# Performance work log

Measured on AMD Instinct MI355X. Metric: run time of the kernel, lower is better.

Reference implementation:

```python
import jax, jax.numpy as jnp
import numpy as np

STAGES = [80, 40, 20]
INPUT = 640
NUM_CLASSES = 80
B = 32
PRE_NMS = 1000      # top-k candidates fed to NMS (fixed-shape surrogate for full sort)
MAX_DET = 100       # max_num_detections
IOU_TH = 0.5
CLASS_OFF = 4096.0  # batched_nms trick: offset boxes per class so classes never overlap


def setup_inputs() -> dict:
    key = jax.random.key(0)
    ks = jax.random.split(key, 6)
    inp = {}
    for i, s in enumerate(STAGES):
        inp[f"cls{i}"] = jax.random.normal(ks[2 * i], (B, NUM_CLASSES, s, s), dtype=jnp.float32)
        # positive ltrb distances, up to ~64 px
        inp[f"box{i}"] = jax.random.uniform(ks[2 * i + 1], (B, 4, s, s), dtype=jnp.float32) * 64.0
    return inp


def _decode_level(cls, box, stage):
    # cls: [B,C,H,W], box: [B,4,H,W]
    step = INPUT // stage
    cls = jax.nn.sigmoid(jnp.transpose(cls, (0, 2, 3, 1)))   # [B,H,W,C]
    conf = jnp.max(cls, axis=-1)                             # [B,H,W]
    cidx = jnp.argmax(cls, axis=-1)                          # [B,H,W]
    box = jnp.transpose(box, (0, 2, 3, 1))                   # [B,H,W,4]
    grid = jnp.arange(stage, dtype=box.dtype) * step
    gx, gy = jnp.meshgrid(grid, grid, indexing='xy')
    block = jnp.stack([gx, gy], axis=-1)                     # [H,W,2]
    xy1 = block - box[..., :2]
    xy2 = block + box[..., 2:4]
    boxes = jnp.concatenate([xy1, xy2], axis=-1).reshape(box.shape[0], -1, 4)
    return boxes, conf.reshape(conf.shape[0], -1), cidx.reshape(cidx.shape[0], -1)


def _iou_matrix(b):
    # b: [N,4] -> [N,N] pairwise IoU
    area = jnp.maximum(b[:, 2] - b[:, 0], 0.) * jnp.maximum(b[:, 3] - b[:, 1], 0.)
    lt = jnp.maximum(b[:, None, :2], b[None, :, :2])
    rb = jnp.minimum(b[:, None, 2:], b[None, :, 2:])
    wh = jnp.maximum(rb - lt, 0.)
    inter = wh[..., 0] * wh[..., 1]
    return inter / (area[:, None] + area[None, :] - inter + 1e-7)


def _nms_image(boxes, scores, classes):
    # class-aware (batched) NMS via per-class coordinate offset
    off = classes.astype(boxes.dtype) * CLASS_OFF
    ob = boxes + off[:, None]
    s_top, idx = jax.lax.top_k(scores, PRE_NMS)
    b_top = ob[idx]                                          # [PRE,4], score-sorted desc
    iou = _iou_matrix(b_top)
    ar = jnp.arange(PRE_NMS)

    def body(i, supp):
        row = (iou[i] > IOU_TH) & (ar > i)
        return jnp.where(supp[i], supp, supp | row)

    supp = jax.lax.fori_loop(0, PRE_NMS, body, jnp.zeros((PRE_NMS,), bool))
    kept_scores = jnp.where(supp, -jnp.inf, s_top)
    sel_s, sel = jax.lax.top_k(kept_scores, MAX_DET)
    final = idx[sel]                                         # indices into original 8400
    valid = jnp.isfinite(sel_s)
    out_b = jnp.where(valid[:, None], boxes[final], 0.)
    out_s = jnp.where(valid, scores[final], 0.)
    out_c = jnp.where(valid, classes[final], -1)
    return out_b, out_s, out_c


def reference(cls0, box0, cls1, box1, cls2, box2):
    parts = [_decode_level(c, b, s) for c, b, s in
             zip([cls0, cls1, cls2], [box0, box1, box2], STAGES)]
    boxes = jnp.concatenate([p[0] for p in parts], axis=1)    # [B,8400,4]
    scores = jnp.concatenate([p[1] for p in parts], axis=1)   # [B,8400]
    classes = jnp.concatenate([p[2] for p in parts], axis=1)  # [B,8400]
    ob, os_, oc = jax.vmap(_nms_image)(boxes, scores, classes)
    boxes_with_scores = jnp.concatenate([ob, os_[..., None]], axis=-1)  # [B,MAX_DET,5]
    return boxes_with_scores, oc
```

## Files before the change

### kernel.cpp

```cpp
#include <hip/hip_runtime.h>

typedef unsigned int u32;
typedef unsigned long long u64;

#define NB 32
#define NCLS 80
#define NANCHOR 8400
#define PRE 1000
#define MAXDET 100
#define NT 1024

__global__ void decode_kernel(const float* __restrict__ cls0, const float* __restrict__ box0,
                              const float* __restrict__ cls1, const float* __restrict__ box1,
                              const float* __restrict__ cls2, const float* __restrict__ box2,
                              float* __restrict__ ws_scores, float4* __restrict__ ws_boxes,
                              int* __restrict__ ws_cls) {
    int g = blockIdx.x * blockDim.x + threadIdx.x;
    if (g >= NB * NANCHOR) return;
    int b = g / NANCHOR;
    int r = g - b * NANCHOR;

    const float* cp; const float* bp;
    int HW, hw, h, w, step;
    if (r < 6400) {
        cp = cls0 + (size_t)b * NCLS * 6400; bp = box0 + (size_t)b * 4 * 6400;
        HW = 6400; hw = r;        h = hw / 80; w = hw - h * 80; step = 8;
    } else if (r < 8000) {
        cp = cls1 + (size_t)b * NCLS * 1600; bp = box1 + (size_t)b * 4 * 1600;
        HW = 1600; hw = r - 6400; h = hw / 40; w = hw - h * 40; step = 16;
    } else {
        cp = cls2 + (size_t)b * NCLS * 400;  bp = box2 + (size_t)b * 4 * 400;
        HW = 400;  hw = r - 8000; h = hw / 20; w = hw - h * 20; step = 32;
    }

    float m = cp[hw];
    int ci = 0;
    for (int c = 1; c < NCLS; ++c) {
        float v = cp[(size_t)c * HW + hw];
        if (v > m) { m = v; ci = c; }
    }
    float score = 1.0f / (1.0f + expf(-m));

    float l = bp[hw], t = bp[HW + hw], rr = bp[2 * HW + hw], bo = bp[3 * HW + hw];
    float gx = (float)(w * step), gy = (float)(h * step);

    ws_scores[g] = score;
    ws_boxes[g] = make_float4(gx - l, gy - t, gx + rr, gy + bo);
    ws_cls[g] = ci;
}

__global__ __launch_bounds__(NT) void nms_kernel(const float* __restrict__ ws_scores,
                                                 const float4* __restrict__ ws_boxes,
                                                 const int* __restrict__ ws_cls,
                                                 float* __restrict__ out) {
    const int b = blockIdx.x;
    const int tid = threadIdx.x;

    __shared__ int s_hist[1024];
    __shared__ u64 s_key[2048];
    __shared__ float s_x1[PRE], s_y1[PRE], s_x2[PRE], s_y2[PRE], s_area[PRE];
    __shared__ int s_supp[PRE];
    __shared__ int s_keep[MAXDET];
    __shared__ int s_C, s_base;
    __shared__ u32 s_thresh;
    __shared__ int s_cnt;

    const float* sc = ws_scores + (size_t)b * NANCHOR;

    s_hist[tid] = 0;
    __syncthreads();
    for (int a = tid; a < NANCHOR; a += NT) {
        u32 sb = __float_as_uint(sc[a]);
        atomicAdd(&s_hist[sb >> 20], 1);
    }
    __syncthreads();
    for (int off = 1; off < 1024; off <<= 1) {
        int v = s_hist[tid];
        int u = (tid + off < 1024) ? s_hist[tid + off] : 0;
        __syncthreads();
        s_hist[tid] = v + u;
        __syncthreads();
    }
    {
        int sfx = s_hist[tid];
        int nxt = (tid < 1023) ? s_hist[tid + 1] : 0;
        if (sfx >= PRE && (tid == 1023 || nxt < PRE)) { s_C = tid; s_base = nxt; }
    }
    __syncthreads();
    const int C = s_C, base = s_base;
    __syncthreads();

    s_hist[tid] = 0;
    __syncthreads();
    for (int a = tid; a < NANCHOR; a += NT) {
        u32 sb = __float_as_uint(sc[a]);
        if ((int)(sb >> 20) == C) atomicAdd(&s_hist[(sb >> 10) & 1023], 1);
    }
    __syncthreads();
    for (int off = 1; off < 1024; off <<= 1) {
        int v = s_hist[tid];
        int u = (tid + off < 1024) ? s_hist[tid + off] : 0;
        __syncthreads();
        s_hist[tid] = v + u;
        __syncthreads();
    }
    {
        int sfx = base + s_hist[tid];
        int nxt = base + ((tid < 1023) ? s_hist[tid + 1] : 0);
        if (sfx >= PRE && (tid == 1023 || nxt < PRE))
            s_thresh = ((u32)C << 20) | ((u32)tid << 10);
    }
    if (tid == 0) s_cnt = 0;
    s_key[tid] = 0ULL;
    s_key[tid + 1024] = 0ULL;
    __syncthreads();
    const u32 thresh = s_thresh;

    for (int a = tid; a < NANCHOR; a += NT) {
        u32 sb = __float_as_uint(sc[a]);
        if (sb >= thresh) {
            int pos = atomicAdd(&s_cnt, 1);
            if (pos < 2048)
                s_key[pos] = ((u64)sb << 14) | (u64)(NANCHOR - 1 - a);
        }
    }
    __syncthreads();

    for (int k = 2; k <= 2048; k <<= 1) {
        for (int j = k >> 1; j > 0; j >>= 1) {
            for (int i = tid; i < 2048; i += NT) {
                int ixj = i ^ j;
                if (ixj > i) {
                    u64 va = s_key[i], vb = s_key[ixj];
                    bool desc = ((i & k) == 0);
                    if (desc ? (va < vb) : (va > vb)) { s_key[i] = vb; s_key[ixj] = va; }
                }
            }
            __syncthreads();
        }
    }

    if (tid < PRE) {
        u64 key = s_key[tid];
        int idx = (NANCHOR - 1) - (int)(key & 16383ULL);
        float4 bx = ws_boxes[(size_t)b * NANCHOR + idx];
        int c = ws_cls[(size_t)b * NANCHOR + idx];
        float off = (float)c * 4096.0f;
        float x1 = bx.x + off, y1 = bx.y + off, x2 = bx.z + off, y2 = bx.w + off;
        s_x1[tid] = x1; s_y1[tid] = y1; s_x2[tid] = x2; s_y2[tid] = y2;
        s_area[tid] = fmaxf(x2 - x1, 0.0f) * fmaxf(y2 - y1, 0.0f);
        s_supp[tid] = 0;
    }
    __syncthreads();

    int nkept = 0;
    for (int i = 0; i < PRE; ++i) {
        if (s_supp[i]) continue;
        if (tid == 0) s_keep[nkept] = i;
        nkept++;
        if (nkept >= MAXDET) break;
        float xi1 = s_x1[i], yi1 = s_y1[i], xi2 = s_x2[i], yi2 = s_y2[i], ai = s_area[i];
        int j = i + 1 + tid;
        if (j < PRE && !s_supp[j]) {
            float lx = fmaxf(xi1, s_x1[j]);
            float ly = fmaxf(yi1, s_y1[j]);
            float rx = fminf(xi2, s_x2[j]);
            float ry = fminf(yi2, s_y2[j]);
            float wx = fmaxf(rx - lx, 0.0f);
            float wy = fmaxf(ry - ly, 0.0f);
            float inter = wx * wy;
            float iou = inter / (ai + s_area[j] - inter + 1e-7f);
            if (iou > 0.5f) s_supp[j] = 1;
        }
        __syncthreads();
    }
    __syncthreads();

    if (tid < MAXDET) {
        float* o = out + ((size_t)b * MAXDET + tid) * 5;
        float* oc = out + (size_t)NB * MAXDET * 5 + (size_t)b * MAXDET + tid;
        if (tid < nkept) {
            int i = s_keep[tid];
            u64 key = s_key[i];
            int idx = (NANCHOR - 1) - (int)(key & 16383ULL);
            float score = __uint_as_float((u32)(key >> 14));
            float4 bx = ws_boxes[(size_t)b * NANCHOR + idx];
            int c = ws_cls[(size_t)b * NANCHOR + idx];
            o[0] = bx.x; o[1] = bx.y; o[2] = bx.z; o[3] = bx.w; o[4] = score;
            *oc = (float)c;
        } else {
            o[0] = 0.0f; o[1] = 0.0f; o[2] = 0.0f; o[3] = 0.0f; o[4] = 0.0f;
            *oc = -1.0f;
        }
    }
}

extern "C" void kernel_launch(void* const* d_in, const int* in_sizes, int n_in,
                              void* d_out, int out_size, void* d_ws, size_t ws_size,
                              hipStream_t stream) {
    const float* cls0 = (const float*)d_in[0];
    const float* box0 = (const float*)d_in[1];
    const float* cls1 = (const float*)d_in[2];
    const float* box1 = (const float*)d_in[3];
    const float* cls2 = (const float*)d_in[4];
    const float* box2 = (const float*)d_in[5];

    float* ws = (float*)d_ws;
    float* ws_scores = ws;
    float4* ws_boxes = (float4*)(ws + NB * NANCHOR);
    int* ws_cls = (int*)(ws + (size_t)NB * NANCHOR * 5);

    int total = NB * NANCHOR;
    decode_kernel<<<(total + 255) / 256, 256, 0, stream>>>(
        cls0, box0, cls1, box1, cls2, box2, ws_scores, ws_boxes, ws_cls);

    nms_kernel<<<NB, NT, 0, stream>>>(ws_scores, ws_boxes, ws_cls, (float*)d_out);
}
```

Baseline: 205.6 us.

## Split decode class reduction across waves and run NMS in one register-resident wave

The decode kernel now gives each 64-anchor group a 256-thread block, with each wave reducing 20 classes before a shared-memory merge. This raises parallelism for the argmax over 80 classes. The NMS kernel drops to 256 threads and keeps scores in registers across the radix-select passes, replacing the log-step block scans with wave-shuffle suffix scans. The greedy suppression loop runs in a single wave with candidate boxes in registers and suppression bits exchanged by shuffles, removing a block barrier per iteration. The trade-off is a smaller block, so the bitonic sort and the other parallel phases do more serial work per thread.

```diff
diff --git a/kernel.cpp b/kernel.cpp
--- a/kernel.cpp
+++ b/kernel.cpp
@@ -8,127 +8,189 @@
 #define NANCHOR 8400
 #define PRE 1000
 #define MAXDET 100
-#define NT 1024
-
-__global__ void decode_kernel(const float* __restrict__ cls0, const float* __restrict__ box0,
-                              const float* __restrict__ cls1, const float* __restrict__ box1,
-                              const float* __restrict__ cls2, const float* __restrict__ box2,
-                              float* __restrict__ ws_scores, float4* __restrict__ ws_boxes,
-                              int* __restrict__ ws_cls) {
-    int g = blockIdx.x * blockDim.x + threadIdx.x;
-    if (g >= NB * NANCHOR) return;
-    int b = g / NANCHOR;
-    int r = g - b * NANCHOR;
+#define NTH 256
+
+__global__ __launch_bounds__(256) void decode_kernel(
+        const float* __restrict__ cls0, const float* __restrict__ box0,
+        const float* __restrict__ cls1, const float* __restrict__ box1,
+        const float* __restrict__ cls2, const float* __restrict__ box2,
+        float* __restrict__ ws_scores, float4* __restrict__ ws_boxes,
+        int* __restrict__ ws_cls) {
+    const int blk = blockIdx.x;
+    const int b = blk / 132;
+    const int ab = blk - b * 132;
+    const int a0 = ab * 64;
+    const int lane = threadIdx.x & 63;
+    const int wv = threadIdx.x >> 6;
 
     const float* cp; const float* bp;
-    int HW, hw, h, w, step;
-    if (r < 6400) {
+    int HW, W, step, hw0;
+    if (a0 < 6400) {
         cp = cls0 + (size_t)b * NCLS * 6400; bp = box0 + (size_t)b * 4 * 6400;
-        HW = 6400; hw = r;        h = hw / 80; w = hw - h * 80; step = 8;
-    } else if (r < 8000) {
+        HW = 6400; W = 80; step = 8;  hw0 = a0;
+    } else if (a0 < 8000) {
         cp = cls1 + (size_t)b * NCLS * 1600; bp = box1 + (size_t)b * 4 * 1600;
-        HW = 1600; hw = r - 6400; h = hw / 40; w = hw - h * 40; step = 16;
+        HW = 1600; W = 40; step = 16; hw0 = a0 - 6400;
     } else {
         cp = cls2 + (size_t)b * NCLS * 400;  bp = box2 + (size_t)b * 4 * 400;
-        HW = 400;  hw = r - 8000; h = hw / 20; w = hw - h * 20; step = 32;
-    }
-
-    float m = cp[hw];
-    int ci = 0;
-    for (int c = 1; c < NCLS; ++c) {
-        float v = cp[(size_t)c * HW + hw];
-        if (v > m) { m = v; ci = c; }
-    }
-    float score = 1.0f / (1.0f + expf(-m));
-
-    float l = bp[hw], t = bp[HW + hw], rr = bp[2 * HW + hw], bo = bp[3 * HW + hw];
-    float gx = (float)(w * step), gy = (float)(h * step);
-
-    ws_scores[g] = score;
-    ws_boxes[g] = make_float4(gx - l, gy - t, gx + rr, gy + bo);
-    ws_cls[g] = ci;
+        HW = 400;  W = 20; step = 32; hw0 = a0 - 8000;
+    }
+
+    const int hw = hw0 + lane;
+    const bool valid = hw < HW;
+
+    __shared__ float s_pm[256];
+    __shared__ int   s_pc[256];
+
+    float m = -1e30f; int ci = 20 * wv;
+    if (valid) {
+        const float* cw = cp + (size_t)(20 * wv) * HW + hw;
+        m = cw[0];
+        #pragma unroll
+        for (int c = 1; c < 20; ++c) {
+            float v = cw[(size_t)c * HW];
+            if (v > m) { m = v; ci = 20 * wv + c; }
+        }
+    }
+    s_pm[threadIdx.x] = m;
+    s_pc[threadIdx.x] = ci;
+    __syncthreads();
+
+    if (threadIdx.x < 64 && valid) {
+        #pragma unroll
+        for (int w = 1; w < 4; ++w) {
+            float v = s_pm[w * 64 + lane];
+            if (v > m) { m = v; ci = s_pc[w * 64 + lane]; }
+        }
+        float score = 1.0f / (1.0f + expf(-m));
+        float l_ = bp[hw], t_ = bp[HW + hw], r_ = bp[2 * HW + hw], bo = bp[3 * HW + hw];
+        int hh = hw / W, ww = hw - hh * W;
+        float gx = (float)(ww * step), gy = (float)(hh * step);
+        int g = b * NANCHOR + a0 + lane;
+        ws_scores[g] = score;
+        ws_boxes[g] = make_float4(gx - l_, gy - t_, gx + r_, gy + bo);
+        ws_cls[g] = ci;
+    }
 }
 
-__global__ __launch_bounds__(NT) void nms_kernel(const float* __restrict__ ws_scores,
-                                                 const float4* __restrict__ ws_boxes,
-                                                 const int* __restrict__ ws_cls,
-                                                 float* __restrict__ out) {
+__device__ __forceinline__ int wave_suffix_incl(int v, int lane) {
+    #pragma unroll
+    for (int off = 1; off < 64; off <<= 1) {
+        int t = __shfl_down(v, off);
+        if (lane + off < 64) v += t;
+    }
+    return v;
+}
+
+__global__ __launch_bounds__(NTH) void nms_kernel(const float* __restrict__ ws_scores,
+                                                  const float4* __restrict__ ws_boxes,
+                                                  const int* __restrict__ ws_cls,
+                                                  float* __restrict__ out) {
     const int b = blockIdx.x;
     const int tid = threadIdx.x;
+    const int lane = tid & 63;
+    const int wv = tid >> 6;
 
     __shared__ int s_hist[1024];
     __shared__ u64 s_key[2048];
-    __shared__ float s_x1[PRE], s_y1[PRE], s_x2[PRE], s_y2[PRE], s_area[PRE];
-    __shared__ int s_supp[PRE];
+    __shared__ float4 s_box[PRE];
+    __shared__ float s_area[PRE];
     __shared__ int s_keep[MAXDET];
+    __shared__ int s_wtot[4];
     __shared__ int s_C, s_base;
     __shared__ u32 s_thresh;
-    __shared__ int s_cnt;
+    __shared__ int s_cnt, s_nkept;
 
     const float* sc = ws_scores + (size_t)b * NANCHOR;
 
-    s_hist[tid] = 0;
-    __syncthreads();
-    for (int a = tid; a < NANCHOR; a += NT) {
-        u32 sb = __float_as_uint(sc[a]);
-        atomicAdd(&s_hist[sb >> 20], 1);
-    }
-    __syncthreads();
-    for (int off = 1; off < 1024; off <<= 1) {
-        int v = s_hist[tid];
-        int u = (tid + off < 1024) ? s_hist[tid + off] : 0;
+    u32 sb[33];
+    #pragma unroll
+    for (int k = 0; k < 33; ++k) {
+        int a = tid + (k << 8);
+        sb[k] = (a < NANCHOR) ? __float_as_uint(sc[a]) : 0u;
+    }
+    *(int4*)&s_hist[4 * tid] = make_int4(0, 0, 0, 0);
+    __syncthreads();
+
+    #pragma unroll
+    for (int k = 0; k < 33; ++k) {
+        int a = tid + (k << 8);
+        if (a < NANCHOR) atomicAdd(&s_hist[sb[k] >> 20], 1);
+    }
+    __syncthreads();
+
+    {
+        int b0 = s_hist[4 * tid], b1 = s_hist[4 * tid + 1], b2 = s_hist[4 * tid + 2], b3 = s_hist[4 * tid + 3];
+        int l3 = b3, l2 = b2 + b3, l1 = b1 + l2, l0 = b0 + l1;
+        int wincl = wave_suffix_incl(l0, lane);
+        if (lane == 0) s_wtot[wv] = wincl;
+        int add = wincl - l0;
         __syncthreads();
-        s_hist[tid] = v + u;
+        #pragma unroll
+        for (int w = 0; w < 4; ++w) if (w > wv) add += s_wtot[w];
+        s_hist[4 * tid] = l0 + add; s_hist[4 * tid + 1] = l1 + add;
+        s_hist[4 * tid + 2] = l2 + add; s_hist[4 * tid + 3] = l3 + add;
         __syncthreads();
     }
+    #pragma unroll
+    for (int k = 0; k < 4; ++k) {
+        int bin = 4 * tid + k;
+        int sfx = s_hist[bin];
+        int nxt = (bin < 1023) ? s_hist[bin + 1] : 0;
+        if (sfx >= PRE && nxt < PRE) { s_C = bin; s_base = nxt; }
+    }
+    __syncthreads();
+    const int C = s_C, base = s_base;
+    *(int4*)&s_hist[4 * tid] = make_int4(0, 0, 0, 0);
+    if (tid == 0) s_cnt = 0;
+    #pragma unroll
+    for (int k = 0; k < 8; ++k) s_key[tid + (k << 8)] = 0ULL;
+    __syncthreads();
+
+    #pragma unroll
+    for (int k = 0; k < 33; ++k) {
+        int a = tid + (k << 8);
+        if (a < NANCHOR && (int)(sb[k] >> 20) == C) atomicAdd(&s_hist[(sb[k] >> 10) & 1023], 1);
+    }
+    __syncthreads();
     {
-        int sfx = s_hist[tid];
-        int nxt = (tid < 1023) ? s_hist[tid + 1] : 0;
-        if (sfx >= PRE && (tid == 1023 || nxt < PRE)) { s_C = tid; s_base = nxt; }
-    }
-    __syncthreads();
-    const int C = s_C, base = s_base;
-    __syncthreads();
-
-    s_hist[tid] = 0;
-    __syncthreads();
-    for (int a = tid; a < NANCHOR; a += NT) {
-        u32 sb = __float_as_uint(sc[a]);
-        if ((int)(sb >> 20) == C) atomicAdd(&s_hist[(sb >> 10) & 1023], 1);
-    }
-    __syncthreads();
-    for (int off = 1; off < 1024; off <<= 1) {
-        int v = s_hist[tid];
-        int u = (tid + off < 1024) ? s_hist[tid + off] : 0;
+        int b0 = s_hist[4 * tid], b1 = s_hist[4 * tid + 1], b2 = s_hist[4 * tid + 2], b3 = s_hist[4 * tid + 3];
+        int l3 = b3, l2 = b2 + b3, l1 = b1 + l2, l0 = b0 + l1;
+        int wincl = wave_suffix_incl(l0, lane);
+        if (lane == 0) s_wtot[wv] = wincl;
+        int add = wincl - l0;
         __syncthreads();
-        s_hist[tid] = v + u;
+        #pragma unroll
+        for (int w = 0; w < 4; ++w) if (w > wv) add += s_wtot[w];
+        s_hist[4 * tid] = l0 + add; s_hist[4 * tid + 1] = l1 + add;
+        s_hist[4 * tid + 2] = l2 + add; s_hist[4 * tid + 3] = l3 + add;
         __syncthreads();
     }
-    {
-        int sfx = base + s_hist[tid];
-        int nxt = base + ((tid < 1023) ? s_hist[tid + 1] : 0);
-        if (sfx >= PRE && (tid == 1023 || nxt < PRE))
-            s_thresh = ((u32)C << 20) | ((u32)tid << 10);
-    }
-    if (tid == 0) s_cnt = 0;
-    s_key[tid] = 0ULL;
-    s_key[tid + 1024] = 0ULL;
-    __syncthreads();
-    const u32 thresh = s_thresh;
-
-    for (int a = tid; a < NANCHOR; a += NT) {
-        u32 sb = __float_as_uint(sc[a]);
-        if (sb >= thresh) {
+    #pragma unroll
+    for (int k = 0; k < 4; ++k) {
+        int f = 4 * tid + k;
+        int full = base + s_hist[f];
+        int nxtf = base + ((f < 1023) ? s_hist[f + 1] : 0);
+        if (full >= PRE && nxtf < PRE) s_thresh = ((u32)C << 20) | ((u32)f << 10);
+    }
+    __syncthreads();
+    const u32 T = s_thresh;
+
+    #pragma unroll
+    for (int k = 0; k < 33; ++k) {
+        int a = tid + (k << 8);
+        if (a < NANCHOR && sb[k] >= T) {
             int pos = atomicAdd(&s_cnt, 1);
             if (pos < 2048)
-                s_key[pos] = ((u64)sb << 14) | (u64)(NANCHOR - 1 - a);
+                s_key[pos] = ((u64)sb[k] << 14) | (u64)(NANCHOR - 1 - a);
         }
     }
     __syncthreads();
 
     for (int k = 2; k <= 2048; k <<= 1) {
         for (int j = k >> 1; j > 0; j >>= 1) {
-            for (int i = tid; i < 2048; i += NT) {
+            #pragma unroll
+            for (int i = tid; i < 2048; i += NTH) {
                 int ixj = i ^ j;
                 if (ixj > i) {
                     u64 va = s_key[i], vb = s_key[ixj];
@@ -140,46 +202,68 @@
         }
     }
 
-    if (tid < PRE) {
-        u64 key = s_key[tid];
+    for (int r = tid; r < PRE; r += NTH) {
+        u64 key = s_key[r];
         int idx = (NANCHOR - 1) - (int)(key & 16383ULL);
         float4 bx = ws_boxes[(size_t)b * NANCHOR + idx];
         int c = ws_cls[(size_t)b * NANCHOR + idx];
         float off = (float)c * 4096.0f;
         float x1 = bx.x + off, y1 = bx.y + off, x2 = bx.z + off, y2 = bx.w + off;
-        s_x1[tid] = x1; s_y1[tid] = y1; s_x2[tid] = x2; s_y2[tid] = y2;
-        s_area[tid] = fmaxf(x2 - x1, 0.0f) * fmaxf(y2 - y1, 0.0f);
-        s_supp[tid] = 0;
-    }
-    __syncthreads();
-
-    int nkept = 0;
-    for (int i = 0; i < PRE; ++i) {
-        if (s_supp[i]) continue;
-        if (tid == 0) s_keep[nkept] = i;
-        nkept++;
-        if (nkept >= MAXDET) break;
-        float xi1 = s_x1[i], yi1 = s_y1[i], xi2 = s_x2[i], yi2 = s_y2[i], ai = s_area[i];
-        int j = i + 1 + tid;
-        if (j < PRE && !s_supp[j]) {
-            float lx = fmaxf(xi1, s_x1[j]);
-            float ly = fmaxf(yi1, s_y1[j]);
-            float rx = fminf(xi2, s_x2[j]);
-            float ry = fminf(yi2, s_y2[j]);
-            float wx = fmaxf(rx - lx, 0.0f);
-            float wy = fmaxf(ry - ly, 0.0f);
-            float inter = wx * wy;
-            float iou = inter / (ai + s_area[j] - inter + 1e-7f);
-            if (iou > 0.5f) s_supp[j] = 1;
-        }
-        __syncthreads();
-    }
-    __syncthreads();
-
+        s_box[r] = make_float4(x1, y1, x2, y2);
+        s_area[r] = fmaxf(x2 - x1, 0.0f) * fmaxf(y2 - y1, 0.0f);
+    }
+    if (tid == 0) s_nkept = 0;
+    __syncthreads();
+
+    if (wv == 0) {
+        float jx1[16], jy1[16], jx2[16], jy2[16], ja[16];
+        #pragma unroll
+        for (int k = 0; k < 16; ++k) {
+            int j = lane + (k << 6);
+            if (j < PRE) {
+                float4 v = s_box[j];
+                jx1[k] = v.x; jy1[k] = v.y; jx2[k] = v.z; jy2[k] = v.w;
+                ja[k] = s_area[j];
+            } else {
+                jx1[k] = 3.0e8f; jy1[k] = 3.0e8f; jx2[k] = 3.0e8f; jy2[k] = 3.0e8f;
+                ja[k] = 0.0f;
+            }
+        }
+        u32 supp = 0;
+        int nkept = 0;
+        for (int i = 0; i < PRE; ++i) {
+            int owner = i & 63, kk = i >> 6;
+            u32 um = (u32)__shfl((int)supp, owner);
+            if ((um >> kk) & 1) continue;
+            if (lane == 0) s_keep[nkept] = i;
+            nkept++;
+            if (nkept >= MAXDET) break;
+            float4 bi = s_box[i];
+            float ai = s_area[i];
+            #pragma unroll
+            for (int k = 0; k < 16; ++k) {
+                int j = lane + (k << 6);
+                bool act = (j > i) && (j < PRE) && !((supp >> k) & 1);
+                float lx = fmaxf(bi.x, jx1[k]);
+                float ly = fmaxf(bi.y, jy1[k]);
+                float rx = fminf(bi.z, jx2[k]);
+                float ry = fminf(bi.w, jy2[k]);
+                float wx = fmaxf(rx - lx, 0.0f);
+                float wy = fmaxf(ry - ly, 0.0f);
+                float inter = wx * wy;
+                float den = ai + ja[k] - inter + 1e-7f;
+                if (act && (inter > 0.5f * den)) supp |= (1u << k);
+            }
+        }
+        if (lane == 0) s_nkept = nkept;
+    }
+    __syncthreads();
+
+    const int nk = s_nkept;
     if (tid < MAXDET) {
         float* o = out + ((size_t)b * MAXDET + tid) * 5;
         float* oc = out + (size_t)NB * MAXDET * 5 + (size_t)b * MAXDET + tid;
-        if (tid < nkept) {
+        if (tid < nk) {
             int i = s_keep[tid];
             u64 key = s_key[i];
             int idx = (NANCHOR - 1) - (int)(key & 16383ULL);
@@ -210,9 +294,8 @@
     float4* ws_boxes = (float4*)(ws + NB * NANCHOR);
     int* ws_cls = (int*)(ws + (size_t)NB * NANCHOR * 5);
 
-    int total = NB * NANCHOR;
-    decode_kernel<<<(total + 255) / 256, 256, 0, stream>>>(
+    decode_kernel<<<NB * 132, 256, 0, stream>>>(
         cls0, box0, cls1, box1, cls2, box2, ws_scores, ws_boxes, ws_cls);
 
-    nms_kernel<<<NB, NT, 0, stream>>>(ws_scores, ws_boxes, ws_cls, (float*)d_out);
+    nms_kernel<<<NB, NTH, 0, stream>>>(ws_scores, ws_boxes, ws_cls, (float*)d_out);
 }
```

Result: slower. 291.4 us (+41.7%).
